# Optimization experiments

Hardware: AMD Instinct MI355X
Metric: run time of the kernel (lower is better)

The kernel has to match this reference:

```python
import jax, jax.numpy as jnp
import numpy as np

N_NODES = 100000
N_EDGES = 1600000
IN_CH, HID_CH, OUT_CH = 128, 128, 64


def _spmm(row, col, val, x, n):
    # COO sparse @ dense: out[r] += val_e * x[col_e]
    gathered = val[:, None] * x[col]  # [E, d]
    return jax.ops.segment_sum(gathered, row, num_segments=n)


def setup_inputs() -> dict:
    key = jax.random.key(0)
    ks = jax.random.split(key, 8)
    x = jax.random.normal(ks[0], (N_NODES, IN_CH), dtype=jnp.float32)
    adj_row = jax.random.randint(ks[1], (N_EDGES,), 0, N_NODES)
    adj_col = jax.random.randint(ks[2], (N_EDGES,), 0, N_NODES)
    adj_val = jax.random.uniform(ks[3], (N_EDGES,), dtype=jnp.float32)
    w1 = jax.random.normal(ks[4], (IN_CH, HID_CH), dtype=jnp.float32) * (1.0 / np.sqrt(IN_CH))
    b1 = jax.random.normal(ks[5], (HID_CH,), dtype=jnp.float32) * 0.01
    w2 = jax.random.normal(ks[6], (HID_CH, OUT_CH), dtype=jnp.float32) * (1.0 / np.sqrt(HID_CH))
    b2 = jax.random.normal(ks[7], (OUT_CH,), dtype=jnp.float32) * 0.01
    return {"x": x, "adj_row": adj_row, "adj_col": adj_col, "adj_val": adj_val,
            "w1": w1, "b1": b1, "w2": w2, "b2": b2}


def reference(x, adj_row, adj_col, adj_val, w1, b1, w2, b2):
    n = x.shape[0]
    # layer 1: spmm -> linear -> relu
    h = _spmm(adj_row, adj_col, adj_val, x, n)
    h = jax.nn.relu(h @ w1 + b1)
    # layer 2: spmm -> linear
    h = _spmm(adj_row, adj_col, adj_val, h, n)
    return h @ w2 + b2
```

## Files before the change

kernel.cpp:

```cpp
#include <hip/hip_runtime.h>


typedef __bf16 v8bf __attribute__((ext_vector_type(8)));
typedef float  v4f  __attribute__((ext_vector_type(4)));

#define MAXB 800

__device__ __forceinline__ unsigned short f2bf(float f) {
    unsigned u = __float_as_uint(f);
    unsigned r = u + 0x7fffu + ((u >> 16) & 1u);
    return (unsigned short)(r >> 16);
}

__global__ __launch_bounds__(256) void hist_prep(const int* __restrict__ arow,
                                                 int* __restrict__ counts, int E, int B,
                                                 const float* __restrict__ w1,
                                                 const float* __restrict__ w2,
                                                 unsigned short* __restrict__ w1T,
                                                 unsigned short* __restrict__ w2T,
                                                 int* __restrict__ rowptr,
                                                 int2* __restrict__ epkS, int N) {
    const int tid = threadIdx.x;
    int gi = blockIdx.x * 256 + tid;
    if (gi < 16384) {
        int n = gi >> 7, k = gi & 127;
        w1T[gi] = f2bf(w1[k * 128 + n]);
    } else if (gi < 24576) {
        int i2 = gi - 16384;
        int n = i2 >> 7, k = i2 & 127;
        w2T[i2] = f2bf(w2[k * 64 + n]);
    } else if (gi < 24576 + 32) {
        epkS[E + (gi - 24576)] = make_int2(0, 0);
    } else if (gi == 24576 + 32) {
        rowptr[N] = E;
    }
    __shared__ int lh[MAXB];
    for (int i = tid; i < B; i += 256) lh[i] = 0;
    __syncthreads();
    const int base = blockIdx.x * 4096;
#pragma unroll
    for (int j = 0; j < 16; ++j) {
        int i = base + j * 256 + tid;
        if (i < E) atomicAdd(&lh[arow[i] >> 7], 1);
    }
    __syncthreads();
    for (int i = tid; i < B; i += 256) {
        int c = lh[i];
        if (c) atomicAdd(&counts[i], c);
    }
}

__global__ __launch_bounds__(256) void scan_s(const int* __restrict__ counts,
                                              int* __restrict__ boff,
                                              int* __restrict__ gcursor, int B, int E) {
    __shared__ int lds[256];
    const int t = threadIdx.x;
    const int b0 = t * 4;
    int v[4];
    int s = 0;
#pragma unroll
    for (int j = 0; j < 4; ++j) {
        v[j] = (b0 + j < B) ? counts[b0 + j] : 0;
        s += v[j];
    }
    lds[t] = s;
    __syncthreads();
    for (int off = 1; off < 256; off <<= 1) {
        int tmp = 0;
        if (t >= off) tmp = lds[t - off];
        __syncthreads();
        if (t >= off) lds[t] += tmp;
        __syncthreads();
    }
    int run = (t > 0) ? lds[t - 1] : 0;
#pragma unroll
    for (int j = 0; j < 4; ++j) {
        if (b0 + j < B) {
            boff[b0 + j] = run;
            gcursor[b0 + j] = run;
        }
        run += v[j];
    }
    if (t == 255) boff[B] = E;
}

__global__ __launch_bounds__(256) void partition_k(const int* __restrict__ arow,
                                                   const int* __restrict__ acol,
                                                   const float* __restrict__ aval,
                                                   int* __restrict__ gcursor,
                                                   int2* __restrict__ epk, int E, int B) {
    __shared__ int2 ldata[4096];
    __shared__ int ldest[4096];
    __shared__ int lhist[MAXB];
    __shared__ int lscan[MAXB];
    __shared__ int ldelta[MAXB];
    __shared__ int lcur[MAXB];
    __shared__ int stmp[256];
    const int tid = threadIdx.x;
    const int base = blockIdx.x * 4096;
    const int cnt = min(4096, E - base);

    for (int i = tid; i < MAXB; i += 256) {
        lhist[i] = 0;
        lcur[i] = 0;
    }
    __syncthreads();

    int rr[16];
#pragma unroll
    for (int j = 0; j < 16; ++j) {
        int i = base + j * 256 + tid;
        rr[j] = (i < E) ? arow[i] : -1;
        if (rr[j] >= 0) atomicAdd(&lhist[rr[j] >> 7], 1);
    }
    __syncthreads();

    const int b0 = tid * 4;
    int v[4];
    int s = 0;
#pragma unroll
    for (int j = 0; j < 4; ++j) {
        v[j] = (b0 + j < MAXB) ? lhist[b0 + j] : 0;
        s += v[j];
    }
    stmp[tid] = s;
    __syncthreads();
    for (int off = 1; off < 256; off <<= 1) {
        int tmp = 0;
        if (tid >= off) tmp = stmp[tid - off];
        __syncthreads();
        if (tid >= off) stmp[tid] += tmp;
        __syncthreads();
    }
    int run = (tid > 0) ? stmp[tid - 1] : 0;
#pragma unroll
    for (int j = 0; j < 4; ++j) {
        if (b0 + j < MAXB) lscan[b0 + j] = run;
        run += v[j];
    }
    __syncthreads();

    for (int b = tid; b < B; b += 256) {
        int c = lhist[b];
        if (c) ldelta[b] = atomicAdd(&gcursor[b], c) - lscan[b];
    }
    __syncthreads();

#pragma unroll
    for (int j = 0; j < 16; ++j) {
        int i = base + j * 256 + tid;
        if (i < E) {
            int r = rr[j];
            int b = r >> 7;
            int lp = atomicAdd(&lcur[b], 1);
            int slot = lscan[b] + lp;
            int pk = acol[i] | ((r & 127) << 17);
            ldata[slot] = make_int2(pk, __float_as_int(aval[i]));
            ldest[slot] = ldelta[b] + slot;
        }
    }
    __syncthreads();

    for (int s2 = tid; s2 < cnt; s2 += 256) epk[ldest[s2]] = ldata[s2];
}

template <int NC, bool AF32>
__device__ __forceinline__ void gemm_body(const void* __restrict__ A,
                                          const unsigned short* __restrict__ wT,
                                          unsigned short* __restrict__ y, int M,
                                          int bid, char* smem) {
    constexpr int KP = 136;
    constexpr int NT = NC / 16;
    unsigned short* wl = (unsigned short*)smem;
    const int tid = threadIdx.x;
    for (int idx = tid; idx < NC * 16; idx += 256) {
        int n = idx >> 4, kc = idx & 15;
        *(uint4*)&wl[n * KP + kc * 8] = *(const uint4*)&wT[n * 128 + kc * 8];
    }
    __syncthreads();

    const int wave = tid >> 6;
    const int lane = tid & 63;
    const int m = lane & 15;
    const int q = lane >> 4;
    const int rowbase = bid * 64 + wave * 16;
    const int rowc = min(rowbase + m, M - 1);

    v4f acc[NT] = {};
    union LU { uint4 qv; v8bf b; };

#pragma unroll
    for (int ks = 0; ks < 4; ++ks) {
        const int k0 = ks * 32 + q * 8;
        v8bf a;
        if (AF32) {
            const float* Ap = (const float*)A + (size_t)rowc * 128 + k0;
            float4 f0 = *(const float4*)Ap;
            float4 f1 = *(const float4*)(Ap + 4);
            union { unsigned short s[8]; v8bf b; } cv;
            cv.s[0] = f2bf(f0.x); cv.s[1] = f2bf(f0.y);
            cv.s[2] = f2bf(f0.z); cv.s[3] = f2bf(f0.w);
            cv.s[4] = f2bf(f1.x); cv.s[5] = f2bf(f1.y);
            cv.s[6] = f2bf(f1.z); cv.s[7] = f2bf(f1.w);
            a = cv.b;
        } else {
            LU lu;
            lu.qv = *(const uint4*)((const unsigned short*)A + (size_t)rowc * 128 + k0);
            a = lu.b;
        }
#pragma unroll
        for (int nt = 0; nt < NT; ++nt) {
            v8bf b = *(const v8bf*)&wl[(nt * 16 + m) * KP + k0];
            acc[nt] = __builtin_amdgcn_mfma_f32_16x16x32_bf16(a, b, acc[nt], 0, 0, 0);
        }
    }
#pragma unroll
    for (int nt = 0; nt < NT; ++nt) {
#pragma unroll
        for (int r = 0; r < 4; ++r) {
            int orow = rowbase + q * 4 + r;
            if (orow < M) y[(size_t)orow * NC + nt * 16 + m] = f2bf(acc[nt][r]);
        }
    }
}

__global__ __launch_bounds__(256) void sort_gemm1(const int* __restrict__ boff,
                                                  const int2* __restrict__ epk,
                                                  int2* __restrict__ epkS,
                                                  int* __restrict__ rowptr, int N, int B,
                                                  const float* __restrict__ x,
                                                  const unsigned short* __restrict__ w1T,
                                                  unsigned short* __restrict__ y1b) {
    __shared__ __align__(16) char smem[34816];
    const int tid = threadIdx.x;
    if (blockIdx.x >= B) {
        gemm_body<128, true>(x, w1T, y1b, N, blockIdx.x - B, smem);
        return;
    }
    int2* sorted = (int2*)smem;
    int*  sc     = (int*)(smem + 32768);
    int*  lcur   = (int*)(smem + 32768 + 512);
    const int b = blockIdx.x;
    const int s = boff[b], e = boff[b + 1];
    const int cnt = min(e - s, 4096);
    if (tid < 128) sc[tid] = 0;
    __syncthreads();
    for (int i = s + tid; i < e; i += 256) {
        int rl = (epk[i].x >> 17) & 127;
        atomicAdd(&sc[rl], 1);
    }
    __syncthreads();
    int hv = (tid < 128) ? sc[tid] : 0;
    for (int off = 1; off < 128; off <<= 1) {
        int add = 0;
        if (tid < 128 && tid >= off) add = sc[tid - off];
        __syncthreads();
        if (tid < 128 && tid >= off) sc[tid] += add;
        __syncthreads();
    }
    if (tid < 128) {
        int ex = sc[tid] - hv;
        lcur[tid] = ex;
        int r = b * 128 + tid;
        if (r < N) rowptr[r] = s + ex;
    }
    __syncthreads();
    for (int i = s + tid; i < e; i += 256) {
        int2 p = epk[i];
        int rl = (p.x >> 17) & 127;
        int slot = atomicAdd(&lcur[rl], 1);
        if (slot < 4096) sorted[slot] = make_int2(p.x & 0x1FFFF, p.y);
    }
    __syncthreads();
    for (int i = tid; i < cnt; i += 256) epkS[s + i] = sorted[i];
}

__global__ __launch_bounds__(256) void spmm_gemm2(const int* __restrict__ rowptr,
                                                  const int2* __restrict__ ep,
                                                  const unsigned short* __restrict__ y1b,
                                                  const float* __restrict__ b1,
                                                  const unsigned short* __restrict__ w2T,
                                                  unsigned short* __restrict__ y2b, int N) {
    constexpr int KP = 136;
    __shared__ unsigned short h1[64 * KP];
    const int tid = threadIdx.x;
    const int wave = tid >> 6, lane = tid & 63;
    const int rowbase = blockIdx.x * 64;
    const unsigned* y32 = (const unsigned*)y1b;
    const float2 bv = ((const float2*)b1)[lane];

    for (int i = 0; i < 16; ++i) {
        const int r = rowbase + wave * 16 + i;
        float accx = 0.f, accy = 0.f;
        if (r < N) {
            const int s = rowptr[r], e = rowptr[r + 1];
            int2 cur[8];
#pragma unroll
            for (int k = 0; k < 8; ++k) cur[k] = ep[s + k];
            for (int j = s; j < e; j += 8) {
                int2 nxt[8];
#pragma unroll
                for (int k = 0; k < 8; ++k) nxt[k] = ep[j + 8 + k];
#pragma unroll
                for (int k = 0; k < 8; ++k) {
                    float v = (j + k < e) ? __int_as_float(cur[k].y) : 0.f;
                    unsigned u = y32[(size_t)cur[k].x * 64 + lane];
                    accx += v * __uint_as_float(u << 16);
                    accy += v * __uint_as_float(u & 0xffff0000u);
                }
#pragma unroll
                for (int k = 0; k < 8; ++k) cur[k] = nxt[k];
            }
        }
        accx = fmaxf(accx + bv.x, 0.f);
        accy = fmaxf(accy + bv.y, 0.f);
        unsigned pk = ((unsigned)f2bf(accy) << 16) | f2bf(accx);
        *(unsigned*)&h1[(wave * 16 + i) * KP + 2 * lane] = pk;
    }
    __syncthreads();

    const int m = lane & 15, q = lane >> 4;
    v4f acc[4] = {};
#pragma unroll
    for (int ks = 0; ks < 4; ++ks) {
        const int k0 = ks * 32 + q * 8;
        v8bf a = *(const v8bf*)&h1[(wave * 16 + m) * KP + k0];
#pragma unroll
        for (int nt = 0; nt < 4; ++nt) {
            v8bf b = *(const v8bf*)&w2T[(nt * 16 + m) * 128 + k0];
            acc[nt] = __builtin_amdgcn_mfma_f32_16x16x32_bf16(a, b, acc[nt], 0, 0, 0);
        }
    }
#pragma unroll
    for (int nt = 0; nt < 4; ++nt) {
#pragma unroll
        for (int r = 0; r < 4; ++r) {
            int orow = rowbase + wave * 16 + q * 4 + r;
            if (orow < N) y2b[(size_t)orow * 64 + nt * 16 + m] = f2bf(acc[nt][r]);
        }
    }
}

__global__ __launch_bounds__(256) void spmm64(const int* __restrict__ rowptr,
                                              const int2* __restrict__ ep,
                                              const unsigned short* __restrict__ yb,
                                              const float* __restrict__ bias,
                                              float* __restrict__ outp, int N) {
    const int row = (blockIdx.x * 256 + threadIdx.x) >> 6;
    const int lane = threadIdx.x & 63;
    if (row >= N) return;
    const int s = rowptr[row], e = rowptr[row + 1];
    float acc = 0.f;
    int2 cur[8];
#pragma unroll
    for (int k = 0; k < 8; ++k) cur[k] = ep[s + k];
    for (int j = s; j < e; j += 8) {
        int2 nxt[8];
#pragma unroll
        for (int k = 0; k < 8; ++k) nxt[k] = ep[j + 8 + k];
#pragma unroll
        for (int k = 0; k < 8; ++k) {
            float v = (j + k < e) ? __int_as_float(cur[k].y) : 0.f;
            unsigned u = yb[(size_t)cur[k].x * 64 + lane];
            acc += v * __uint_as_float(u << 16);
        }
#pragma unroll
        for (int k = 0; k < 8; ++k) cur[k] = nxt[k];
    }
    acc += bias[lane];
    outp[(size_t)row * 64 + lane] = acc;
}

extern "C" void kernel_launch(void* const* d_in, const int* in_sizes, int n_in,
                              void* d_out, int out_size, void* d_ws, size_t ws_size,
                              hipStream_t stream) {
    const float* x    = (const float*)d_in[0];
    const int*   arow = (const int*)d_in[1];
    const int*   acol = (const int*)d_in[2];
    const float* aval = (const float*)d_in[3];
    const float* w1   = (const float*)d_in[4];
    const float* b1   = (const float*)d_in[5];
    const float* w2   = (const float*)d_in[6];
    const float* b2   = (const float*)d_in[7];
    float*       out  = (float*)d_out;

    const int N = in_sizes[0] / 128;
    const int E = in_sizes[1];
    const int B = (N + 127) >> 7;

    char* p = (char*)d_ws;
    auto alloc = [&](size_t bytes) {
        char* r = p;
        p += (bytes + 255) & ~(size_t)255;
        return r;
    };
    int*            counts  = (int*)alloc((size_t)MAXB * 4);
    int*            boff    = (int*)alloc((size_t)(MAXB + 1) * 4);
    int*            gcursor = (int*)alloc((size_t)MAXB * 4);
    int*            rowptr  = (int*)alloc((size_t)(N + 1) * 4);
    int2*           epkS    = (int2*)alloc((size_t)(E + 32) * 8);
    unsigned short* w1T     = (unsigned short*)alloc(128 * 128 * 2);
    unsigned short* w2T     = (unsigned short*)alloc(64 * 128 * 2);
    unsigned short* y1b     = (unsigned short*)alloc((size_t)N * 128 * 2);
    int2*           epk     = (int2*)alloc((size_t)E * 8);
    unsigned short* y2b     = (unsigned short*)alloc((size_t)N * 64 * 2);

    const int gemm_blocks = (N + 63) / 64;
    const int pb = (E + 4095) / 4096;

    hipMemsetAsync(counts, 0, (size_t)MAXB * 4, stream);
    hist_prep<<<pb, 256, 0, stream>>>(arow, counts, E, B, w1, w2, w1T, w2T,
                                      rowptr, epkS, N);
    scan_s<<<1, 256, 0, stream>>>(counts, boff, gcursor, B, E);
    partition_k<<<pb, 256, 0, stream>>>(arow, acol, aval, gcursor, epk, E, B);
    sort_gemm1<<<B + gemm_blocks, 256, 0, stream>>>(boff, epk, epkS, rowptr, N, B,
                                                    x, w1T, y1b);
    spmm_gemm2<<<gemm_blocks, 256, 0, stream>>>(rowptr, epkS, y1b, b1, w2T, y2b, N);
    const int spmm_blocks = (N + 3) / 4;
    spmm64<<<spmm_blocks, 256, 0, stream>>>(rowptr, epkS, y2b, b2, out, N);
}
```

Before: 321.6 us.

## Gather several edges per wave with 16-byte loads and shuffle-reduce partial sums

Both SpMM kernels now split each wave into edge slots. Each lane loads a 16-byte chunk (8 bf16 values) of a neighbor row instead of one 32-bit or 16-bit element, so a single wave processes 4 or 8 edges at once. Partial sums are combined with xor shuffles, and a few lanes write the biased, packed output with vector stores. Row bounds are read via readfirstlane and reused across consecutive rows. The aim is fewer, wider memory transactions and more edges in flight, at the cost of extra shuffle-reduction work and idle lanes during the final write.

```diff
diff --git a/kernel.cpp b/kernel.cpp
--- a/kernel.cpp
+++ b/kernel.cpp
@@ -285,37 +285,74 @@
     __shared__ unsigned short h1[64 * KP];
     const int tid = threadIdx.x;
     const int wave = tid >> 6, lane = tid & 63;
+    const int eslot = lane >> 4;
+    const int cb = lane & 15;
     const int rowbase = blockIdx.x * 64;
     const unsigned* y32 = (const unsigned*)y1b;
-    const float2 bv = ((const float2*)b1)[lane];
-
+    const float4 bb0 = *(const float4*)&b1[8 * cb];
+    const float4 bb1 = *(const float4*)&b1[8 * cb + 4];
+
+    const int r0 = rowbase + wave * 16;
+    int e_prev = (r0 < N) ? __builtin_amdgcn_readfirstlane(rowptr[r0]) : 0;
     for (int i = 0; i < 16; ++i) {
-        const int r = rowbase + wave * 16 + i;
-        float accx = 0.f, accy = 0.f;
+        const int r = r0 + i;
+        float a[8] = {0.f, 0.f, 0.f, 0.f, 0.f, 0.f, 0.f, 0.f};
         if (r < N) {
-            const int s = rowptr[r], e = rowptr[r + 1];
-            int2 cur[8];
-#pragma unroll
-            for (int k = 0; k < 8; ++k) cur[k] = ep[s + k];
-            for (int j = s; j < e; j += 8) {
-                int2 nxt[8];
-#pragma unroll
-                for (int k = 0; k < 8; ++k) nxt[k] = ep[j + 8 + k];
-#pragma unroll
-                for (int k = 0; k < 8; ++k) {
-                    float v = (j + k < e) ? __int_as_float(cur[k].y) : 0.f;
-                    unsigned u = y32[(size_t)cur[k].x * 64 + lane];
-                    accx += v * __uint_as_float(u << 16);
-                    accy += v * __uint_as_float(u & 0xffff0000u);
+            const int s = e_prev;
+            const int e = __builtin_amdgcn_readfirstlane(rowptr[r + 1]);
+            e_prev = e;
+            int2 cur[4];
+#pragma unroll
+            for (int k = 0; k < 4; ++k) cur[k] = ep[s + 4 * k + eslot];
+            for (int j = s; j < e; j += 16) {
+                int2 nxt[4];
+#pragma unroll
+                for (int k = 0; k < 4; ++k) nxt[k] = ep[j + 16 + 4 * k + eslot];
+                uint4 g[4];
+                float v[4];
+#pragma unroll
+                for (int k = 0; k < 4; ++k) {
+                    v[k] = (j + 4 * k + eslot < e) ? __int_as_float(cur[k].y) : 0.f;
+                    if (j + 4 * k < e)
+                        g[k] = *(const uint4*)(y32 + (((unsigned)cur[k].x) << 6) + (cb << 2));
+                    else
+                        g[k] = make_uint4(0u, 0u, 0u, 0u);
                 }
 #pragma unroll
-                for (int k = 0; k < 8; ++k) cur[k] = nxt[k];
+                for (int k = 0; k < 4; ++k) {
+                    a[0] += v[k] * __uint_as_float(g[k].x << 16);
+                    a[1] += v[k] * __uint_as_float(g[k].x & 0xffff0000u);
+                    a[2] += v[k] * __uint_as_float(g[k].y << 16);
+                    a[3] += v[k] * __uint_as_float(g[k].y & 0xffff0000u);
+                    a[4] += v[k] * __uint_as_float(g[k].z << 16);
+                    a[5] += v[k] * __uint_as_float(g[k].z & 0xffff0000u);
+                    a[6] += v[k] * __uint_as_float(g[k].w << 16);
+                    a[7] += v[k] * __uint_as_float(g[k].w & 0xffff0000u);
+                }
+#pragma unroll
+                for (int k = 0; k < 4; ++k) cur[k] = nxt[k];
             }
         }
-        accx = fmaxf(accx + bv.x, 0.f);
-        accy = fmaxf(accy + bv.y, 0.f);
-        unsigned pk = ((unsigned)f2bf(accy) << 16) | f2bf(accx);
-        *(unsigned*)&h1[(wave * 16 + i) * KP + 2 * lane] = pk;
+#pragma unroll
+        for (int t = 0; t < 8; ++t) a[t] += __shfl_xor(a[t], 16);
+#pragma unroll
+        for (int t = 0; t < 8; ++t) a[t] += __shfl_xor(a[t], 32);
+        if (lane < 16) {
+            float f0 = fmaxf(a[0] + bb0.x, 0.f);
+            float f1 = fmaxf(a[1] + bb0.y, 0.f);
+            float f2 = fmaxf(a[2] + bb0.z, 0.f);
+            float f3 = fmaxf(a[3] + bb0.w, 0.f);
+            float f4 = fmaxf(a[4] + bb1.x, 0.f);
+            float f5 = fmaxf(a[5] + bb1.y, 0.f);
+            float f6 = fmaxf(a[6] + bb1.z, 0.f);
+            float f7 = fmaxf(a[7] + bb1.w, 0.f);
+            uint4 pk;
+            pk.x = ((unsigned)f2bf(f1) << 16) | f2bf(f0);
+            pk.y = ((unsigned)f2bf(f3) << 16) | f2bf(f2);
+            pk.z = ((unsigned)f2bf(f5) << 16) | f2bf(f4);
+            pk.w = ((unsigned)f2bf(f7) << 16) | f2bf(f6);
+            *(uint4*)&h1[(wave * 16 + i) * KP + 8 * cb] = pk;
+        }
     }
     __syncthreads();
 
@@ -324,11 +361,11 @@
 #pragma unroll
     for (int ks = 0; ks < 4; ++ks) {
         const int k0 = ks * 32 + q * 8;
-        v8bf a = *(const v8bf*)&h1[(wave * 16 + m) * KP + k0];
+        v8bf av = *(const v8bf*)&h1[(wave * 16 + m) * KP + k0];
 #pragma unroll
         for (int nt = 0; nt < 4; ++nt) {
             v8bf b = *(const v8bf*)&w2T[(nt * 16 + m) * 128 + k0];
-            acc[nt] = __builtin_amdgcn_mfma_f32_16x16x32_bf16(a, b, acc[nt], 0, 0, 0);
+            acc[nt] = __builtin_amdgcn_mfma_f32_16x16x32_bf16(av, b, acc[nt], 0, 0, 0);
         }
     }
 #pragma unroll
@@ -349,26 +386,58 @@
     const int row = (blockIdx.x * 256 + threadIdx.x) >> 6;
     const int lane = threadIdx.x & 63;
     if (row >= N) return;
-    const int s = rowptr[row], e = rowptr[row + 1];
-    float acc = 0.f;
-    int2 cur[8];
-#pragma unroll
-    for (int k = 0; k < 8; ++k) cur[k] = ep[s + k];
-    for (int j = s; j < e; j += 8) {
-        int2 nxt[8];
-#pragma unroll
-        for (int k = 0; k < 8; ++k) nxt[k] = ep[j + 8 + k];
-#pragma unroll
-        for (int k = 0; k < 8; ++k) {
-            float v = (j + k < e) ? __int_as_float(cur[k].y) : 0.f;
-            unsigned u = yb[(size_t)cur[k].x * 64 + lane];
-            acc += v * __uint_as_float(u << 16);
-        }
-#pragma unroll
-        for (int k = 0; k < 8; ++k) cur[k] = nxt[k];
-    }
-    acc += bias[lane];
-    outp[(size_t)row * 64 + lane] = acc;
+    const int eslot = lane >> 3;
+    const int cb = lane & 7;
+    const unsigned* y32 = (const unsigned*)yb;
+    const int s = __builtin_amdgcn_readfirstlane(rowptr[row]);
+    const int e = __builtin_amdgcn_readfirstlane(rowptr[row + 1]);
+    float a[8] = {0.f, 0.f, 0.f, 0.f, 0.f, 0.f, 0.f, 0.f};
+    int2 cur[2];
+#pragma unroll
+    for (int k = 0; k < 2; ++k) cur[k] = ep[s + 8 * k + eslot];
+    for (int j = s; j < e; j += 16) {
+        int2 nxt[2];
+#pragma unroll
+        for (int k = 0; k < 2; ++k) nxt[k] = ep[j + 16 + 8 * k + eslot];
+        uint4 g[2];
+        float v[2];
+#pragma unroll
+        for (int k = 0; k < 2; ++k) {
+            v[k] = (j + 8 * k + eslot < e) ? __int_as_float(cur[k].y) : 0.f;
+            if (j + 8 * k < e)
+                g[k] = *(const uint4*)(y32 + (((unsigned)cur[k].x) << 5) + (cb << 2));
+            else
+                g[k] = make_uint4(0u, 0u, 0u, 0u);
+        }
+#pragma unroll
+        for (int k = 0; k < 2; ++k) {
+            a[0] += v[k] * __uint_as_float(g[k].x << 16);
+            a[1] += v[k] * __uint_as_float(g[k].x & 0xffff0000u);
+            a[2] += v[k] * __uint_as_float(g[k].y << 16);
+            a[3] += v[k] * __uint_as_float(g[k].y & 0xffff0000u);
+            a[4] += v[k] * __uint_as_float(g[k].z << 16);
+            a[5] += v[k] * __uint_as_float(g[k].z & 0xffff0000u);
+            a[6] += v[k] * __uint_as_float(g[k].w << 16);
+            a[7] += v[k] * __uint_as_float(g[k].w & 0xffff0000u);
+        }
+#pragma unroll
+        for (int k = 0; k < 2; ++k) cur[k] = nxt[k];
+    }
+#pragma unroll
+    for (int t = 0; t < 8; ++t) a[t] += __shfl_xor(a[t], 8);
+#pragma unroll
+    for (int t = 0; t < 8; ++t) a[t] += __shfl_xor(a[t], 16);
+#pragma unroll
+    for (int t = 0; t < 8; ++t) a[t] += __shfl_xor(a[t], 32);
+    if (lane < 8) {
+        const float4 c0 = *(const float4*)&bias[8 * cb];
+        const float4 c1 = *(const float4*)&bias[8 * cb + 4];
+        float4 o0 = make_float4(a[0] + c0.x, a[1] + c0.y, a[2] + c0.z, a[3] + c0.w);
+        float4 o1 = make_float4(a[4] + c1.x, a[5] + c1.y, a[6] + c1.z, a[7] + c1.w);
+        float* op = outp + (size_t)row * 64 + 8 * cb;
+        *(float4*)op = o0;
+        *(float4*)(op + 4) = o1;
+    }
 }
 
 extern "C" void kernel_launch(void* const* d_in, const int* in_sizes, int n_in,
```

Measured after the change: 290.9 us. 1.11x faster.
